# Optimization experiments

Measured on AMD Instinct MI355X. Metric: run time of the kernel, lower is better.

The kernel has to match this reference:

```python
import jax, jax.numpy as jnp
import numpy as np

B, T, D = 2, 4096, 4096
H, HKV = 32, 8
DH = D // H  # 128
EPS = 1e-5
ROPE_BASE = 10000.0


def rmsnorm(x, gamma):
    var = jnp.mean(x * x, axis=-1, keepdims=True)
    return x * jax.lax.rsqrt(var + EPS) * gamma


def rope(x):
    # x: (n, h, t, d) -- rotary applied over last dim, interleaved pairs
    d, t = x.shape[-1], x.shape[-2]
    inv_freq = 1.0 / (ROPE_BASE ** (jnp.arange(0, d, 2, dtype=jnp.float32) / d))
    ang = jnp.arange(t, dtype=jnp.float32)[:, None] * inv_freq[None, :]  # (t, d/2)
    cos, sin = jnp.cos(ang), jnp.sin(ang)
    x1, x2 = x[..., 0::2], x[..., 1::2]
    r1 = x1 * cos - x2 * sin
    r2 = x1 * sin + x2 * cos
    return jnp.stack([r1, r2], axis=-1).reshape(x.shape)


def setup_inputs() -> dict:
    key = jax.random.key(0)
    ks = jax.random.split(key, 4)
    s_in = 1.0 / np.sqrt(D)
    x = jax.random.normal(ks[0], (B, T, D), dtype=jnp.float32)
    Wq = jax.random.normal(ks[1], (D, D), dtype=jnp.float32) * s_in
    Wk = jax.random.normal(ks[2], (D, HKV * DH), dtype=jnp.float32) * s_in
    Wv = jax.random.normal(ks[3], (D, HKV * DH), dtype=jnp.float32) * s_in
    gq = jnp.ones((D,), dtype=jnp.float32)
    gk = jnp.ones((HKV * DH,), dtype=jnp.float32)
    return {"x": x, "Wq": Wq, "Wk": Wk, "Wv": Wv, "gq": gq, "gk": gk}


def reference(x, Wq, Wk, Wv, gq, gk):
    n, t, _ = x.shape
    q = rmsnorm(x @ Wq, gq)
    k = rmsnorm(x @ Wk, gk)
    v = x @ Wv
    # (n, t, h, dh) -> (n, h, t, dh)
    q = q.reshape(n, t, H, DH).transpose(0, 2, 1, 3)
    k = k.reshape(n, t, HKV, DH).transpose(0, 2, 1, 3)
    v = v.reshape(n, t, HKV, DH).transpose(0, 2, 1, 3)
    q = rope(q)
    k = rope(k)
    n_rep = H // HKV
    k = jnp.repeat(k, n_rep, axis=1)  # repeat_interleave over head dim
    v = jnp.repeat(v, n_rep, axis=1)
    return q, k, v
```

## Files before the change

### kernel.cpp

```cpp
#include <hip/hip_runtime.h>
#include <hip/hip_bf16.h>
#include <stdint.h>

#define HS     524288UL
#define KBASE  33554432UL
#define VBASE  67108864UL
#define EPSq   1e-5f

typedef unsigned short u16;
typedef unsigned int   u32;
typedef __attribute__((ext_vector_type(8))) __bf16 bf16x8;
typedef __attribute__((ext_vector_type(4))) float  f32x4;

typedef __attribute__((address_space(3))) u32* lds_u32p;
typedef const __attribute__((address_space(1))) u32* g_u32p;

__device__ __forceinline__ void g2lds16(const void* g, void* lds) {
    __builtin_amdgcn_global_load_lds((g_u32p)(uintptr_t)g, (lds_u32p)(uintptr_t)lds, 16, 0, 0);
}
__device__ __forceinline__ u16 f2bf(float f) {
    __hip_bfloat16 h = __float2bfloat16(f);
    return __builtin_bit_cast(u16, h);
}

__device__ __forceinline__ size_t wt_row_off(int n, int mode) {
    if (mode == 0) return (size_t)n * 4096;
    int c = n >> 8;
    int head = (c / 3) * 4 + (c % 3) + 1;
    return 2 * (KBASE + (size_t)head * HS) + (size_t)(n & 255) * 4096;
}

__global__ __launch_bounds__(256) void convert_x(const float4* __restrict__ x,
                                                 ushort4* __restrict__ xb) {
    int i = blockIdx.x * 256 + threadIdx.x;
    for (int g = i; g < 8388608; g += gridDim.x * 256) {
        float4 v = x[g];
        ushort4 o;
        o.x = f2bf(v.x); o.y = f2bf(v.y); o.z = f2bf(v.z); o.w = f2bf(v.w);
        xb[g] = o;
    }
}

__global__ __launch_bounds__(256) void transpose_w(
    const float* Wq, const float* Wk, const float* Wv, u16* wt, int mode)
{
    __shared__ u16 tile[64][65];
    const int n0 = blockIdx.x * 64;
    const int k0 = blockIdx.y * 64;
    const float* src; int ldn, c0;
    if (n0 < 4096)      { src = Wq; ldn = 4096; c0 = n0; }
    else if (n0 < 5120) { src = Wk; ldn = 1024; c0 = n0 - 4096; }
    else                { src = Wv; ldn = 1024; c0 = n0 - 5120; }
    const int tx = threadIdx.x & 63, ty = threadIdx.x >> 6;
#pragma unroll
    for (int r = 0; r < 16; ++r) {
        int kr = r * 4 + ty;
        tile[tx][kr] = f2bf(src[(size_t)(k0 + kr) * ldn + c0 + tx]);
    }
    __syncthreads();
#pragma unroll
    for (int r = 0; r < 16; ++r) {
        int nr = r * 4 + ty;
        wt[wt_row_off(n0 + nr, mode) + k0 + tx] = tile[nr][tx];
    }
}

__global__ __launch_bounds__(256) void gemm_qkv(
    const u16* xb, const u16* wt, float* out, int mode)
{
    __shared__ u16 Al[128 * 32];
    __shared__ u16 Bl[128 * 32];

    const int tid  = threadIdx.x;
    const int lane = tid & 63;
    const int wave = tid >> 6;
    const int m0   = blockIdx.x * 128;
    const int n0   = blockIdx.y * 128;

    const int ch0 = wave * 128 + lane;
    const int ch1 = ch0 + 64;
    const u16* gA0 = xb + (size_t)(m0 + (ch0 >> 2)) * 4096 + (ch0 & 3) * 8;
    const u16* gA1 = xb + (size_t)(m0 + (ch1 >> 2)) * 4096 + (ch1 & 3) * 8;
    const size_t wtrow = wt_row_off(n0, mode);
    const u16* gB0 = wt + wtrow + (size_t)(ch0 >> 2) * 4096 + (ch0 & 3) * 8;
    const u16* gB1 = wt + wtrow + (size_t)(ch1 >> 2) * 4096 + (ch1 & 3) * 8;

    u16* lA0 = &Al[(wave * 2 + 0) * 512];
    u16* lA1 = &Al[(wave * 2 + 1) * 512];
    u16* lB0 = &Bl[(wave * 2 + 0) * 512];
    u16* lB1 = &Bl[(wave * 2 + 1) * 512];

    const int wm = wave >> 1, wn = wave & 1;
    const int col16 = lane & 15, quad = lane >> 4;
    const int aoff = (wm * 64 + col16) * 32 + quad * 8;
    const int boff = (wn * 64 + col16) * 32 + quad * 8;

    f32x4 acc[4][4];
#pragma unroll
    for (int mt = 0; mt < 4; ++mt)
#pragma unroll
        for (int nt = 0; nt < 4; ++nt)
            acc[mt][nt] = (f32x4)0.0f;

    for (int kt = 0; kt < 128; ++kt) {
        if (kt) __syncthreads();
        g2lds16(gA0, lA0);
        g2lds16(gA1, lA1);
        g2lds16(gB0, lB0);
        g2lds16(gB1, lB1);
        gA0 += 32; gA1 += 32; gB0 += 32; gB1 += 32;
        __syncthreads();

        bf16x8 a[4], b[4];
#pragma unroll
        for (int mt = 0; mt < 4; ++mt)
            a[mt] = *(const bf16x8*)&Al[aoff + mt * 16 * 32];
#pragma unroll
        for (int nt = 0; nt < 4; ++nt)
            b[nt] = *(const bf16x8*)&Bl[boff + nt * 16 * 32];
#pragma unroll
        for (int mt = 0; mt < 4; ++mt)
#pragma unroll
            for (int nt = 0; nt < 4; ++nt)
                acc[mt][nt] = __builtin_amdgcn_mfma_f32_16x16x32_bf16(
                    a[mt], b[nt], acc[mt][nt], 0, 0, 0);
    }

    const int b_idx = m0 >> 12;
    const int tbase = m0 & 4095;
    size_t headbase; int nslots = 1;
    if (n0 < 4096) {
        headbase = (size_t)(b_idx * 32 + (n0 >> 7)) * HS;
    } else if (n0 < 5120) {
        headbase = KBASE + (size_t)(b_idx * 32 + ((n0 - 4096) >> 7) * 4) * HS;
    } else {
        headbase = VBASE + (size_t)(b_idx * 32 + ((n0 - 5120) >> 7) * 4) * HS;
        nslots = 4;
    }
    const int dcol = wn * 64 + col16;
#pragma unroll
    for (int mt = 0; mt < 4; ++mt) {
#pragma unroll
        for (int r = 0; r < 4; ++r) {
            int mlocal = wm * 64 + mt * 16 + quad * 4 + r;
            size_t rowb = headbase + (size_t)(tbase + mlocal) * 128;
#pragma unroll
            for (int nt = 0; nt < 4; ++nt) {
                float val = acc[mt][nt][r];
                size_t addr = rowb + dcol + nt * 16;
                out[addr] = val;
                if (nslots == 4) {
                    out[addr + HS]     = val;
                    out[addr + 2 * HS] = val;
                    out[addr + 3 * HS] = val;
                }
            }
        }
    }
}

__global__ __launch_bounds__(256) void finalize_qk(
    float* out, const float* gq, const float* gk)
{
    const int bt = blockIdx.x;
    const int b  = bt >> 12, t = bt & 4095;
    const int tid = threadIdx.x;

    float qv[8][2], kv[2][2];
    float ssq = 0.f, ssk = 0.f;
#pragma unroll
    for (int j = 0; j < 8; ++j) {
        int p = j * 256 + tid;
        int head = p >> 6, i = p & 63;
        size_t a = (size_t)(b * 32 + head) * HS + (size_t)t * 128 + 2 * i;
        float2 u = *(const float2*)(out + a);
        qv[j][0] = u.x; qv[j][1] = u.y;
        ssq += u.x * u.x + u.y * u.y;
    }
#pragma unroll
    for (int j = 0; j < 2; ++j) {
        int p = j * 256 + tid;
        int hk = p >> 6, i = p & 63;
        size_t a = KBASE + (size_t)(b * 32 + hk * 4) * HS + (size_t)t * 128 + 2 * i;
        float2 u = *(const float2*)(out + a);
        kv[j][0] = u.x; kv[j][1] = u.y;
        ssk += u.x * u.x + u.y * u.y;
    }
#pragma unroll
    for (int off = 32; off; off >>= 1) {
        ssq += __shfl_xor(ssq, off, 64);
        ssk += __shfl_xor(ssk, off, 64);
    }
    __shared__ float red[2][4];
    if ((tid & 63) == 0) { red[0][tid >> 6] = ssq; red[1][tid >> 6] = ssk; }
    __syncthreads();
    const float sq = red[0][0] + red[0][1] + red[0][2] + red[0][3];
    const float sk = red[1][0] + red[1][1] + red[1][2] + red[1][3];
    const float qs = rsqrtf(sq * (1.f / 4096.f) + EPSq);
    const float ks = rsqrtf(sk * (1.f / 1024.f) + EPSq);
    const float tf = (float)t;
    const float LN1E4_64 = 0.14391156831f;

#pragma unroll
    for (int j = 0; j < 8; ++j) {
        int p = j * 256 + tid;
        int head = p >> 6, i = p & 63;
        float ang = tf * __expf(-(float)i * LN1E4_64);
        float s, c; sincosf(ang, &s, &c);
        float2 g = *(const float2*)(gq + head * 128 + 2 * i);
        float x1 = qv[j][0] * qs * g.x;
        float x2 = qv[j][1] * qs * g.y;
        float2 o; o.x = x1 * c - x2 * s; o.y = x1 * s + x2 * c;
        size_t a = (size_t)(b * 32 + head) * HS + (size_t)t * 128 + 2 * i;
        *(float2*)(out + a) = o;
    }
#pragma unroll
    for (int j = 0; j < 2; ++j) {
        int p = j * 256 + tid;
        int hk = p >> 6, i = p & 63;
        float ang = tf * __expf(-(float)i * LN1E4_64);
        float s, c; sincosf(ang, &s, &c);
        float2 g = *(const float2*)(gk + hk * 128 + 2 * i);
        float x1 = kv[j][0] * ks * g.x;
        float x2 = kv[j][1] * ks * g.y;
        float2 o; o.x = x1 * c - x2 * s; o.y = x1 * s + x2 * c;
        size_t a = KBASE + (size_t)(b * 32 + hk * 4) * HS + (size_t)t * 128 + 2 * i;
        *(float2*)(out + a) = o;
        *(float2*)(out + a + HS) = o;
        *(float2*)(out + a + 2 * HS) = o;
        *(float2*)(out + a + 3 * HS) = o;
    }
}

__global__ __launch_bounds__(256) void gemm_f32(
    const float* x, const float* Wq, const float* Wk, const float* Wv, float* out)
{
    __shared__ float As[16][65], Bs[16][65];
    const int m0 = blockIdx.x * 64;
    const int c0 = blockIdx.y * 64;
    const float* W; int ldn, nc0;
    if (c0 < 4096)      { W = Wq; ldn = 4096; nc0 = c0; }
    else if (c0 < 5120) { W = Wk; ldn = 1024; nc0 = c0 - 4096; }
    else                { W = Wv; ldn = 1024; nc0 = c0 - 5120; }
    const int tid = threadIdx.x, tx = tid & 15, ty = tid >> 4;
    float acc[4][4] = {};
    for (int k0 = 0; k0 < 4096; k0 += 16) {
        __syncthreads();
#pragma unroll
        for (int l = 0; l < 4; ++l) {
            int idx = l * 256 + tid;
            int m = idx >> 4, k = idx & 15;
            As[k][m] = x[(size_t)(m0 + m) * 4096 + k0 + k];
        }
#pragma unroll
        for (int l = 0; l < 4; ++l) {
            int idx = l * 256 + tid;
            int k = idx >> 6, n = idx & 63;
            Bs[k][n] = W[(size_t)(k0 + k) * ldn + nc0 + n];
        }
        __syncthreads();
#pragma unroll
        for (int k = 0; k < 16; ++k) {
            float a[4], bb[4];
#pragma unroll
            for (int i = 0; i < 4; ++i) { a[i] = As[k][ty * 4 + i]; bb[i] = Bs[k][tx * 4 + i]; }
#pragma unroll
            for (int i = 0; i < 4; ++i)
#pragma unroll
                for (int j = 0; j < 4; ++j) acc[i][j] += a[i] * bb[j];
        }
    }
    const int b = m0 >> 12, tbase = m0 & 4095;
#pragma unroll
    for (int i = 0; i < 4; ++i) {
#pragma unroll
        for (int j = 0; j < 4; ++j) {
            int m = ty * 4 + i, c = c0 + tx * 4 + j;
            float v = acc[i][j];
            size_t addr; int ns = 1;
            if (c < 4096) {
                addr = (size_t)(b * 32 + (c >> 7)) * HS + (size_t)(tbase + m) * 128 + (c & 127);
            } else if (c < 5120) {
                addr = KBASE + (size_t)(b * 32 + ((c - 4096) >> 7) * 4) * HS
                     + (size_t)(tbase + m) * 128 + ((c - 4096) & 127);
            } else {
                addr = VBASE + (size_t)(b * 32 + ((c - 5120) >> 7) * 4) * HS
                     + (size_t)(tbase + m) * 128 + ((c - 5120) & 127);
                ns = 4;
            }
            out[addr] = v;
            if (ns == 4) { out[addr + HS] = v; out[addr + 2 * HS] = v; out[addr + 3 * HS] = v; }
        }
    }
}

extern "C" void kernel_launch(void* const* d_in, const int* in_sizes, int n_in,
                              void* d_out, int out_size, void* d_ws, size_t ws_size,
                              hipStream_t stream)
{
    const float* x  = (const float*)d_in[0];
    const float* Wq = (const float*)d_in[1];
    const float* Wk = (const float*)d_in[2];
    const float* Wv = (const float*)d_in[3];
    const float* gq = (const float*)d_in[4];
    const float* gk = (const float*)d_in[5];
    float* out = (float*)d_out;

    const size_t xb_bytes = 8192ULL * 4096ULL * 2ULL;
    const size_t wt_bytes = 6144ULL * 4096ULL * 2ULL;
    dim3 tb(256);

    if (ws_size >= xb_bytes) {
        u16* xb = (u16*)d_ws;
        u16* wt; int mode;
        if (ws_size >= xb_bytes + wt_bytes) { wt = (u16*)((char*)d_ws + xb_bytes); mode = 0; }
        else                                { wt = (u16*)d_out; mode = 1; }
        convert_x  <<<dim3(2048),    tb, 0, stream>>>((const float4*)x, (ushort4*)xb);
        transpose_w<<<dim3(96, 64),  tb, 0, stream>>>(Wq, Wk, Wv, wt, mode);
        gemm_qkv   <<<dim3(64, 48),  tb, 0, stream>>>(xb, wt, out, mode);
    } else {
        gemm_f32   <<<dim3(128, 96), tb, 0, stream>>>(x, Wq, Wk, Wv, out);
    }
    finalize_qk<<<dim3(8192), tb, 0, stream>>>(out, gq, gk);
}
```

Before: 1.058 ms.

## Rewrite QKV GEMM as 256x256 tile double-buffered pipelined kernel with swizzled LDS

The bf16 QKV GEMM now uses 256x256 output tiles with 512 threads (8 waves) and a BK=64 double-buffered LDS pipeline. Global-to-LDS async loads are interleaved with MFMA phases using explicit barriers, vmcnt waits and s_setprio. LDS rows get an XOR swizzle to avoid bank conflicts, and block indices are remapped for L2 locality. The goal is to hide memory latency and raise MFMA utilization, at the cost of higher register and LDS pressure and fragile hand-scheduled synchronization.

```diff
diff --git a/kernel.cpp b/kernel.cpp
--- a/kernel.cpp
+++ b/kernel.cpp
@@ -65,89 +65,157 @@
     }
 }
 
-__global__ __launch_bounds__(256) void gemm_qkv(
+#define SBAR()  do { asm volatile("" ::: "memory"); __builtin_amdgcn_s_barrier(); \
+                     asm volatile("" ::: "memory"); } while (0)
+#define LGKM0() asm volatile("s_waitcnt lgkmcnt(0)" ::: "memory")
+#define VMC(n)  asm volatile("s_waitcnt vmcnt(" #n ")" ::: "memory")
+#define CFENCE() asm volatile("" ::: "memory")
+
+__global__ __launch_bounds__(512, 2) void gemm_qkv(
     const u16* xb, const u16* wt, float* out, int mode)
 {
-    __shared__ u16 Al[128 * 32];
-    __shared__ u16 Bl[128 * 32];
+    __shared__ u16 Lt[2][4][8192];
 
     const int tid  = threadIdx.x;
     const int lane = tid & 63;
     const int wave = tid >> 6;
-    const int m0   = blockIdx.x * 128;
-    const int n0   = blockIdx.y * 128;
-
-    const int ch0 = wave * 128 + lane;
-    const int ch1 = ch0 + 64;
-    const u16* gA0 = xb + (size_t)(m0 + (ch0 >> 2)) * 4096 + (ch0 & 3) * 8;
-    const u16* gA1 = xb + (size_t)(m0 + (ch1 >> 2)) * 4096 + (ch1 & 3) * 8;
-    const size_t wtrow = wt_row_off(n0, mode);
-    const u16* gB0 = wt + wtrow + (size_t)(ch0 >> 2) * 4096 + (ch0 & 3) * 8;
-    const u16* gB1 = wt + wtrow + (size_t)(ch1 >> 2) * 4096 + (ch1 & 3) * 8;
-
-    u16* lA0 = &Al[(wave * 2 + 0) * 512];
-    u16* lA1 = &Al[(wave * 2 + 1) * 512];
-    u16* lB0 = &Bl[(wave * 2 + 0) * 512];
-    u16* lB1 = &Bl[(wave * 2 + 1) * 512];
-
-    const int wm = wave >> 1, wn = wave & 1;
+
+    const int swz = (blockIdx.x & 7) * 96 + (blockIdx.x >> 3);
+    const int m0  = (swz & 31) * 256;
+    const int n0  = (swz >> 5) * 256;
+
+    const int srow  = wave * 16 + (lane >> 3);
+    const int sslot = (lane & 7) ^ (lane >> 3);
+    const size_t wtb = wt_row_off(n0, mode);
+    const u16* p0a = xb + (size_t)(m0 + srow)       * 4096 + sslot * 8;
+    const u16* p0b = xb + (size_t)(m0 + srow + 8)   * 4096 + sslot * 8;
+    const u16* p1a = xb + (size_t)(m0 + 128 + srow)     * 4096 + sslot * 8;
+    const u16* p1b = xb + (size_t)(m0 + 128 + srow + 8) * 4096 + sslot * 8;
+    const u16* p2a = wt + wtb + (size_t)(srow)       * 4096 + sslot * 8;
+    const u16* p2b = wt + wtb + (size_t)(srow + 8)   * 4096 + sslot * 8;
+    const u16* p3a = wt + wtb + (size_t)(128 + srow)     * 4096 + sslot * 8;
+    const u16* p3b = wt + wtb + (size_t)(128 + srow + 8) * 4096 + sslot * 8;
+    const int dst0 = wave * 1024;
+
+#define STAGE(buf, sec) do { \
+    g2lds16(p##sec##a, &Lt[buf][sec][dst0]);       p##sec##a += 64; \
+    g2lds16(p##sec##b, &Lt[buf][sec][dst0 + 512]); p##sec##b += 64; \
+} while (0)
+
+    const int wm = wave >> 2, wn = wave & 3;
     const int col16 = lane & 15, quad = lane >> 4;
-    const int aoff = (wm * 64 + col16) * 32 + quad * 8;
-    const int boff = (wn * 64 + col16) * 32 + quad * 8;
-
-    f32x4 acc[4][4];
-#pragma unroll
-    for (int mt = 0; mt < 4; ++mt)
-#pragma unroll
-        for (int nt = 0; nt < 4; ++nt)
-            acc[mt][nt] = (f32x4)0.0f;
-
-    for (int kt = 0; kt < 128; ++kt) {
-        if (kt) __syncthreads();
-        g2lds16(gA0, lA0);
-        g2lds16(gA1, lA1);
-        g2lds16(gB0, lB0);
-        g2lds16(gB1, lB1);
-        gA0 += 32; gA1 += 32; gB0 += 32; gB1 += 32;
-        __syncthreads();
-
-        bf16x8 a[4], b[4];
-#pragma unroll
-        for (int mt = 0; mt < 4; ++mt)
-            a[mt] = *(const bf16x8*)&Al[aoff + mt * 16 * 32];
-#pragma unroll
-        for (int nt = 0; nt < 4; ++nt)
-            b[nt] = *(const bf16x8*)&Bl[boff + nt * 16 * 32];
-#pragma unroll
-        for (int mt = 0; mt < 4; ++mt)
-#pragma unroll
-            for (int nt = 0; nt < 4; ++nt)
-                acc[mt][nt] = __builtin_amdgcn_mfma_f32_16x16x32_bf16(
-                    a[mt], b[nt], acc[mt][nt], 0, 0, 0);
-    }
+    const int sl0 = (quad ^ (col16 & 7)) * 8;
+    const int sl1 = sl0 ^ 32;
+
+    bf16x8 a[2][4];
+    bf16x8 bb[2][2][2];
+    f32x4  acc[8][4];
+#pragma unroll
+    for (int i = 0; i < 8; ++i)
+#pragma unroll
+        for (int j = 0; j < 4; ++j) acc[i][j] = (f32x4)0.0f;
+
+#define READ_A(buf, mq) do { \
+    _Pragma("unroll") \
+    for (int mf2 = 0; mf2 < 4; ++mf2) { \
+        const u16* _p = &Lt[buf][wm][((mq) * 64 + mf2 * 16 + col16) * 64]; \
+        a[0][mf2] = *(const bf16x8*)(_p + sl0); \
+        a[1][mf2] = *(const bf16x8*)(_p + sl1); \
+    } \
+} while (0)
+
+#define READ_B(buf, nh) do { \
+    _Pragma("unroll") \
+    for (int nf2 = 0; nf2 < 2; ++nf2) { \
+        const u16* _p = &Lt[buf][2 + (wn >> 1)] \
+                          [((wn & 1) * 64 + (nh) * 32 + nf2 * 16 + col16) * 64]; \
+        bb[nh][0][nf2] = *(const bf16x8*)(_p + sl0); \
+        bb[nh][1][nf2] = *(const bf16x8*)(_p + sl1); \
+    } \
+} while (0)
+
+#define MMA(mq, nh) do { \
+    __builtin_amdgcn_s_setprio(1); \
+    _Pragma("unroll") \
+    for (int mf2 = 0; mf2 < 4; ++mf2) \
+    _Pragma("unroll") \
+    for (int nf2 = 0; nf2 < 2; ++nf2) { \
+        acc[(mq)*4+mf2][(nh)*2+nf2] = __builtin_amdgcn_mfma_f32_16x16x32_bf16( \
+            a[0][mf2], bb[nh][0][nf2], acc[(mq)*4+mf2][(nh)*2+nf2], 0, 0, 0); \
+        acc[(mq)*4+mf2][(nh)*2+nf2] = __builtin_amdgcn_mfma_f32_16x16x32_bf16( \
+            a[1][mf2], bb[nh][1][nf2], acc[(mq)*4+mf2][(nh)*2+nf2], 0, 0, 0); \
+    } \
+    __builtin_amdgcn_s_setprio(0); \
+} while (0)
+
+    STAGE(0, 2); STAGE(0, 3); STAGE(0, 0); STAGE(0, 1);
+    CFENCE();
+    STAGE(1, 2); STAGE(1, 3); STAGE(1, 0);
+    VMC(6);
+    SBAR();
+
+    for (int it = 0; it < 31; ++it) {
+        READ_A(0, 0); READ_B(0, 0); STAGE(1, 1);
+        SBAR(); LGKM0(); MMA(0, 0); SBAR();
+        READ_B(0, 1); STAGE(0, 2);
+        SBAR(); LGKM0(); MMA(0, 1); SBAR();
+        READ_A(0, 1); STAGE(0, 3);
+        SBAR(); LGKM0(); MMA(1, 1); SBAR();
+        STAGE(0, 0);
+        SBAR(); LGKM0(); MMA(1, 0); VMC(6); SBAR();
+        READ_A(1, 0); READ_B(1, 0); STAGE(0, 1);
+        SBAR(); LGKM0(); MMA(0, 0); SBAR();
+        READ_B(1, 1); STAGE(1, 2);
+        SBAR(); LGKM0(); MMA(0, 1); SBAR();
+        READ_A(1, 1); STAGE(1, 3);
+        SBAR(); LGKM0(); MMA(1, 1); SBAR();
+        STAGE(1, 0);
+        SBAR(); LGKM0(); MMA(1, 0); VMC(6); SBAR();
+    }
+
+    READ_A(0, 0); READ_B(0, 0); STAGE(1, 1);
+    SBAR(); LGKM0(); MMA(0, 0); SBAR();
+    READ_B(0, 1);
+    SBAR(); LGKM0(); MMA(0, 1); SBAR();
+    READ_A(0, 1);
+    SBAR(); LGKM0(); MMA(1, 1); SBAR();
+    SBAR(); LGKM0(); MMA(1, 0); VMC(0); SBAR();
+    READ_A(1, 0); READ_B(1, 0);
+    SBAR(); LGKM0(); MMA(0, 0); SBAR();
+    READ_B(1, 1);
+    SBAR(); LGKM0(); MMA(0, 1); SBAR();
+    READ_A(1, 1);
+    SBAR(); LGKM0(); MMA(1, 1); SBAR();
+    SBAR(); LGKM0(); MMA(1, 0);
+
+#undef STAGE
+#undef READ_A
+#undef READ_B
+#undef MMA
 
     const int b_idx = m0 >> 12;
     const int tbase = m0 & 4095;
+    const int ng0   = n0 + wn * 64;
     size_t headbase; int nslots = 1;
-    if (n0 < 4096) {
-        headbase = (size_t)(b_idx * 32 + (n0 >> 7)) * HS;
-    } else if (n0 < 5120) {
-        headbase = KBASE + (size_t)(b_idx * 32 + ((n0 - 4096) >> 7) * 4) * HS;
+    if (ng0 < 4096) {
+        headbase = (size_t)(b_idx * 32 + (ng0 >> 7)) * HS;
+    } else if (ng0 < 5120) {
+        headbase = KBASE + (size_t)(b_idx * 32 + ((ng0 - 4096) >> 7) * 4) * HS;
     } else {
-        headbase = VBASE + (size_t)(b_idx * 32 + ((n0 - 5120) >> 7) * 4) * HS;
+        headbase = VBASE + (size_t)(b_idx * 32 + ((ng0 - 5120) >> 7) * 4) * HS;
         nslots = 4;
     }
-    const int dcol = wn * 64 + col16;
-#pragma unroll
-    for (int mt = 0; mt < 4; ++mt) {
+    const int c0 = (ng0 & 127) + col16;
+#pragma unroll
+    for (int mf = 0; mf < 8; ++mf) {
 #pragma unroll
         for (int r = 0; r < 4; ++r) {
-            int mlocal = wm * 64 + mt * 16 + quad * 4 + r;
+            int mlocal = wm * 128 + mf * 16 + quad * 4 + r;
             size_t rowb = headbase + (size_t)(tbase + mlocal) * 128;
 #pragma unroll
-            for (int nt = 0; nt < 4; ++nt) {
-                float val = acc[mt][nt][r];
-                size_t addr = rowb + dcol + nt * 16;
+            for (int nf = 0; nf < 4; ++nf) {
+                float val = acc[mf][nf][r];
+                size_t addr = rowb + c0 + nf * 16;
                 out[addr] = val;
                 if (nslots == 4) {
                     out[addr + HS]     = val;
@@ -261,13 +329,13 @@
         __syncthreads();
 #pragma unroll
         for (int k = 0; k < 16; ++k) {
-            float a[4], bb[4];
-#pragma unroll
-            for (int i = 0; i < 4; ++i) { a[i] = As[k][ty * 4 + i]; bb[i] = Bs[k][tx * 4 + i]; }
+            float a[4], bbv[4];
+#pragma unroll
+            for (int i = 0; i < 4; ++i) { a[i] = As[k][ty * 4 + i]; bbv[i] = Bs[k][tx * 4 + i]; }
 #pragma unroll
             for (int i = 0; i < 4; ++i)
 #pragma unroll
-                for (int j = 0; j < 4; ++j) acc[i][j] += a[i] * bb[j];
+                for (int j = 0; j < 4; ++j) acc[i][j] += a[i] * bbv[j];
         }
     }
     const int b = m0 >> 12, tbase = m0 & 4095;
@@ -317,7 +385,7 @@
         else                                { wt = (u16*)d_out; mode = 1; }
         convert_x  <<<dim3(2048),    tb, 0, stream>>>((const float4*)x, (ushort4*)xb);
         transpose_w<<<dim3(96, 64),  tb, 0, stream>>>(Wq, Wk, Wv, wt, mode);
-        gemm_qkv   <<<dim3(64, 48),  tb, 0, stream>>>(xb, wt, out, mode);
+        gemm_qkv   <<<dim3(768), dim3(512), 0, stream>>>(xb, wt, out, mode);
     } else {
         gemm_f32   <<<dim3(128, 96), tb, 0, stream>>>(x, Wq, Wk, Wv, out);
     }
```

Result: faster. 1.024 ms (-3.2%).
